# Performance work log

Measured on AMD Instinct MI355X. Metric: run time of the kernel, lower is better.

Reference implementation:

```python
import jax, jax.numpy as jnp
import numpy as np

EPS = 1e-12  # F.normalize eps


def setup_inputs() -> dict:
    key = jax.random.key(0)
    B, T, D = 1024, 32, 1024
    inputs = jax.random.normal(key, (B, T, D), dtype=jnp.float32)
    return {"inputs": inputs}


def reference(inputs) -> jnp.ndarray:
    # L2-normalize each frame embedding along D (torch F.normalize, p=2, dim=2)
    norm = jnp.maximum(jnp.linalg.norm(inputs, axis=2, keepdims=True), EPS)
    inputs_normed = inputs / norm                     # [B, T, D]
    mean_rep = jnp.mean(inputs_normed, axis=1)        # [B, D]
    # Original loops over T computing matmul(...).diag(); equivalent to a
    # per-sample dot product of each frame with its own clip mean.
    dots = jnp.einsum("btd,bd->bt", inputs_normed, mean_rep)  # [B, T]
    dist = jnp.sum(1.0 - dots, axis=1)                # [B]
    return jnp.mean(dist)
```

## Files before the change

### kernel.cpp

```cpp
#include <hip/hip_runtime.h>


#define TT 32
#define DD 1024
#define BB 1024

__global__ __launch_bounds__(512, 4) void clip_partial_kernel(
    const float* __restrict__ x, float* __restrict__ partial) {
  const int b = blockIdx.x;
  const float* __restrict__ xb = x + (size_t)b * (TT * DD);

  const int lane = threadIdx.x & 63;
  const int wave = threadIdx.x >> 6;

  __shared__ float4 sacc[8 * 4 * 64];
  __shared__ float wsum[4];

  float4 v[4][4];
#pragma unroll
  for (int r = 0; r < 4; ++r) {
    const int t = wave * 4 + r;
#pragma unroll
    for (int i = 0; i < 4; ++i)
      v[r][i] = *reinterpret_cast<const float4*>(xb + t * DD + i * 256 +
                                                 lane * 4);
  }

  float inv[4];
#pragma unroll
  for (int r = 0; r < 4; ++r) {
    float ss = 0.0f;
#pragma unroll
    for (int i = 0; i < 4; ++i)
      ss += v[r][i].x * v[r][i].x + v[r][i].y * v[r][i].y +
            v[r][i].z * v[r][i].z + v[r][i].w * v[r][i].w;
#pragma unroll
    for (int off = 32; off; off >>= 1) ss += __shfl_xor(ss, off);
    inv[r] = 1.0f / fmaxf(sqrtf(ss), 1e-12f);
  }

#pragma unroll
  for (int i = 0; i < 4; ++i) {
    float4 a = make_float4(0.f, 0.f, 0.f, 0.f);
#pragma unroll
    for (int r = 0; r < 4; ++r) {
      a.x = fmaf(v[r][i].x, inv[r], a.x);
      a.y = fmaf(v[r][i].y, inv[r], a.y);
      a.z = fmaf(v[r][i].z, inv[r], a.z);
      a.w = fmaf(v[r][i].w, inv[r], a.w);
    }
    sacc[(wave * 4 + i) * 64 + lane] = a;
  }
  __syncthreads();

  float local = 0.0f;
  if (threadIdx.x < 256) {
    const int i = threadIdx.x >> 6;
    float4 s = make_float4(0.f, 0.f, 0.f, 0.f);
#pragma unroll
    for (int w = 0; w < 8; ++w) {
      const float4 t4 = sacc[(w * 4 + i) * 64 + lane];
      s.x += t4.x;
      s.y += t4.y;
      s.z += t4.z;
      s.w += t4.w;
    }
    local = s.x * s.x + s.y * s.y + s.z * s.z + s.w * s.w;
  }
#pragma unroll
  for (int off = 32; off; off >>= 1) local += __shfl_xor(local, off);
  if (wave < 4 && lane == 0) wsum[wave] = local;
  __syncthreads();
  if (threadIdx.x == 0) {
    const float s2 = wsum[0] + wsum[1] + wsum[2] + wsum[3];
    partial[b] = (float)TT - s2 * (1.0f / (float)TT);
  }
}

__global__ __launch_bounds__(256) void clip_reduce_kernel(
    const float* __restrict__ partial, float* __restrict__ out) {
  const int lane = threadIdx.x & 63;
  const int wave = threadIdx.x >> 6;
  const float4 v =
      *reinterpret_cast<const float4*>(partial + threadIdx.x * 4);
  float s = v.x + v.y + v.z + v.w;
#pragma unroll
  for (int off = 32; off; off >>= 1) s += __shfl_xor(s, off);
  __shared__ float wsum[4];
  if (lane == 0) wsum[wave] = s;
  __syncthreads();
  if (threadIdx.x == 0)
    out[0] = (wsum[0] + wsum[1] + wsum[2] + wsum[3]) * (1.0f / (float)BB);
}

extern "C" void kernel_launch(void* const* d_in, const int* in_sizes, int n_in,
                              void* d_out, int out_size, void* d_ws,
                              size_t ws_size, hipStream_t stream) {
  const float* x = (const float*)d_in[0];
  float* partial = (float*)d_ws;
  float* out = (float*)d_out;

  clip_partial_kernel<<<BB, 512, 0, stream>>>(x, partial);
  clip_reduce_kernel<<<1, 256, 0, stream>>>(partial, out);
}
```

Measured before the change: 27.93 us.

## Fuse partial and final reduction into cooperative kernel with prefetching of second clip

Replaces the two-launch scheme with one cooperative kernel of 512 blocks. Each block processes two clips and issues the loads for the second clip while reducing the first. A grid-wide sync then lets block 0 compute the final mean, removing the second kernel launch. The trade-off is grid-sync overhead, cooperative-launch requirements, and higher register pressure from the prefetch. If the cooperative launch fails, the code falls back to the original two kernels.

```diff
diff --git a/kernel.cpp b/kernel.cpp
--- a/kernel.cpp
+++ b/kernel.cpp
@@ -1,15 +1,127 @@
 #include <hip/hip_runtime.h>
+#include <hip/hip_cooperative_groups.h>
+
+namespace cg = cooperative_groups;
 
 
 #define TT 32
 #define DD 1024
 #define BB 1024
+#define GRID 512
+
+__global__ __launch_bounds__(512, 4) void clip_fused_kernel(
+    const float* __restrict__ x, float* __restrict__ partial,
+    float* __restrict__ out) {
+  const int lane = threadIdx.x & 63;
+  const int wave = threadIdx.x >> 6;
+
+  __shared__ float4 sacc[8 * 4 * 64];
+  __shared__ float wsum[4];
+  __shared__ float w2[8];
+
+  const int b0 = blockIdx.x;
+  const int b1 = blockIdx.x + GRID;
+
+  float4 v[4][4];
+  {
+    const float* __restrict__ xb = x + (size_t)b0 * (TT * DD);
+#pragma unroll
+    for (int r = 0; r < 4; ++r)
+#pragma unroll
+      for (int i = 0; i < 4; ++i)
+        v[r][i] = *reinterpret_cast<const float4*>(
+            xb + (wave * 4 + r) * DD + i * 256 + lane * 4);
+  }
+
+#pragma unroll
+  for (int s = 0; s < 2; ++s) {
+    const int b = (s == 0) ? b0 : b1;
+
+    float inv[4];
+#pragma unroll
+    for (int r = 0; r < 4; ++r) {
+      float ss = 0.0f;
+#pragma unroll
+      for (int i = 0; i < 4; ++i)
+        ss += v[r][i].x * v[r][i].x + v[r][i].y * v[r][i].y +
+              v[r][i].z * v[r][i].z + v[r][i].w * v[r][i].w;
+#pragma unroll
+      for (int off = 32; off; off >>= 1) ss += __shfl_xor(ss, off);
+      inv[r] = 1.0f / fmaxf(sqrtf(ss), 1e-12f);
+    }
+
+    float4 a[4];
+#pragma unroll
+    for (int i = 0; i < 4; ++i) {
+      a[i] = make_float4(0.f, 0.f, 0.f, 0.f);
+#pragma unroll
+      for (int r = 0; r < 4; ++r) {
+        a[i].x = fmaf(v[r][i].x, inv[r], a[i].x);
+        a[i].y = fmaf(v[r][i].y, inv[r], a[i].y);
+        a[i].z = fmaf(v[r][i].z, inv[r], a[i].z);
+        a[i].w = fmaf(v[r][i].w, inv[r], a[i].w);
+      }
+    }
+
+    if (s == 0) {
+      const float* __restrict__ xb1 = x + (size_t)b1 * (TT * DD);
+#pragma unroll
+      for (int r = 0; r < 4; ++r)
+#pragma unroll
+        for (int i = 0; i < 4; ++i)
+          v[r][i] = *reinterpret_cast<const float4*>(
+              xb1 + (wave * 4 + r) * DD + i * 256 + lane * 4);
+    }
+
+#pragma unroll
+    for (int i = 0; i < 4; ++i) sacc[(wave * 4 + i) * 64 + lane] = a[i];
+    __syncthreads();
+
+    float local = 0.0f;
+    if (threadIdx.x < 256) {
+      const int i = threadIdx.x >> 6;
+      float4 t4s = make_float4(0.f, 0.f, 0.f, 0.f);
+#pragma unroll
+      for (int w = 0; w < 8; ++w) {
+        const float4 t4 = sacc[(w * 4 + i) * 64 + lane];
+        t4s.x += t4.x;
+        t4s.y += t4.y;
+        t4s.z += t4.z;
+        t4s.w += t4.w;
+      }
+      local = t4s.x * t4s.x + t4s.y * t4s.y + t4s.z * t4s.z + t4s.w * t4s.w;
+    }
+#pragma unroll
+    for (int off = 32; off; off >>= 1) local += __shfl_xor(local, off);
+    if (wave < 4 && lane == 0) wsum[wave] = local;
+    __syncthreads();
+    if (threadIdx.x == 0) {
+      const float s2 = wsum[0] + wsum[1] + wsum[2] + wsum[3];
+      partial[b] = (float)TT - s2 * (1.0f / (float)TT);
+    }
+  }
+
+  cg::this_grid().sync();
+  if (blockIdx.x == 0) {
+    float sred = partial[threadIdx.x] + partial[threadIdx.x + 512];
+#pragma unroll
+    for (int off = 32; off; off >>= 1) sred += __shfl_xor(sred, off);
+    if (lane == 0) w2[wave] = sred;
+    __syncthreads();
+    if (threadIdx.x == 0) {
+      float tot = 0.0f;
+#pragma unroll
+      for (int i = 0; i < 8; ++i) tot += w2[i];
+      out[0] = tot * (1.0f / (float)BB);
+    }
+  }
+}
+
 
 __global__ __launch_bounds__(512, 4) void clip_partial_kernel(
     const float* __restrict__ x, float* __restrict__ partial) {
   const int b = blockIdx.x;
   const float* __restrict__ xb = x + (size_t)b * (TT * DD);
-
   const int lane = threadIdx.x & 63;
   const int wave = threadIdx.x >> 6;
 
@@ -18,13 +130,11 @@
 
   float4 v[4][4];
 #pragma unroll
-  for (int r = 0; r < 4; ++r) {
-    const int t = wave * 4 + r;
+  for (int r = 0; r < 4; ++r)
 #pragma unroll
     for (int i = 0; i < 4; ++i)
-      v[r][i] = *reinterpret_cast<const float4*>(xb + t * DD + i * 256 +
-                                                 lane * 4);
-  }
+      v[r][i] = *reinterpret_cast<const float4*>(xb + (wave * 4 + r) * DD +
+                                                 i * 256 + lane * 4);
 
   float inv[4];
 #pragma unroll
@@ -56,16 +166,16 @@
   float local = 0.0f;
   if (threadIdx.x < 256) {
     const int i = threadIdx.x >> 6;
-    float4 s = make_float4(0.f, 0.f, 0.f, 0.f);
+    float4 s4 = make_float4(0.f, 0.f, 0.f, 0.f);
 #pragma unroll
     for (int w = 0; w < 8; ++w) {
       const float4 t4 = sacc[(w * 4 + i) * 64 + lane];
-      s.x += t4.x;
-      s.y += t4.y;
-      s.z += t4.z;
-      s.w += t4.w;
-    }
-    local = s.x * s.x + s.y * s.y + s.z * s.z + s.w * s.w;
+      s4.x += t4.x;
+      s4.y += t4.y;
+      s4.z += t4.z;
+      s4.w += t4.w;
+    }
+    local = s4.x * s4.x + s4.y * s4.y + s4.z * s4.z + s4.w * s4.w;
   }
 #pragma unroll
   for (int off = 32; off; off >>= 1) local += __shfl_xor(local, off);
@@ -100,6 +210,12 @@
   float* partial = (float*)d_ws;
   float* out = (float*)d_out;
 
-  clip_partial_kernel<<<BB, 512, 0, stream>>>(x, partial);
-  clip_reduce_kernel<<<1, 256, 0, stream>>>(partial, out);
-}
+  void* args[] = {(void*)&x, (void*)&partial, (void*)&out};
+  hipError_t err = hipLaunchCooperativeKernel(
+      reinterpret_cast<void*>(clip_fused_kernel), dim3(GRID), dim3(512), args,
+      0, stream);
+  if (err != hipSuccess) {
+    clip_partial_kernel<<<BB, 512, 0, stream>>>(x, partial);
+    clip_reduce_kernel<<<1, 256, 0, stream>>>(partial, out);
+  }
+}
```

Result: slower. 93.70 us (+235.5%).
